# Kernel optimization log

Measured on AMD Instinct MI355X. Metric: run time of the kernel, lower is better.

## Reference

```python
import jax, jax.numpy as jnp
import numpy as np

B, T, HID = 4, 2048, 1024
H, FD, HD = 16, 16, 64          # heads, feature_dim, head_dim
CHUNK = 64                      # chunk size for chunked linear attention
EPS_LN = 1e-5                   # layer-norm eps inside feature map
EPS_Z = 1e-10                   # normalize_output eps


def setup_inputs() -> dict:
    key = jax.random.key(0)
    ks = jax.random.split(key, 7)
    init = lambda k, shp: jax.random.normal(k, shp, jnp.float32) * (shp[-1] ** -0.5)
    return {
        "hidden_states": jax.random.normal(ks[0], (B, T, HID), jnp.float32),
        "Wq": init(ks[1], (H * FD, HID)),     # q_proj weight [out,in], no bias
        "Wk": init(ks[2], (H * FD, HID)),
        "Wv": init(ks[3], (H * HD, HID)),
        "Wo": init(ks[4], (H * HD, HID)),
        "gamma": jnp.ones((FD,), jnp.float32),  # RebasedFeatureMap layer-norm scale
        "beta": jnp.zeros((FD,), jnp.float32),  # RebasedFeatureMap layer-norm shift
    }


def _feature_map(x, gamma, beta):
    # layer_norm over feature_dim, then quadratic (outer-product) feature map.
    mu = x.mean(-1, keepdims=True)
    var = ((x - mu) ** 2).mean(-1, keepdims=True)
    xn = (x - mu) * jax.lax.rsqrt(var + EPS_LN) * gamma + beta
    d = xn.shape[-1]
    # [B,T,H,d] -> [B,T,H,d*d]
    x2 = (xn[..., :, None] * xn[..., None, :]).reshape(*xn.shape[:-1], d * d)
    return x2 * (d ** -0.5)


def _chunk_linear_attn(q, k, v):
    # Chunk-recurrent causal linear attention (simple GLA with no gates, scale=1).
    Bq, Tq, Hq, Kq = q.shape
    Vd = v.shape[-1]
    N = Tq // CHUNK
    # [B,T,H,D] -> [N,B,H,C,D] for scan over chunks
    to_chunks = lambda x: x.reshape(Bq, N, CHUNK, Hq, x.shape[-1]).transpose(1, 0, 3, 2, 4)
    qc, kc, vc = to_chunks(q), to_chunks(k), to_chunks(v)
    mask = jnp.tril(jnp.ones((CHUNK, CHUNK), bool))

    def step(state, xs):
        qb, kb, vb = xs  # [B,H,C,K], [B,H,C,K], [B,H,C,V]
        att = jnp.einsum('bhik,bhjk->bhij', qb, kb)
        att = jnp.where(mask, att, 0.0)
        o = jnp.einsum('bhij,bhjv->bhiv', att, vb) + jnp.einsum('bhik,bhkv->bhiv', qb, state)
        state = state + jnp.einsum('bhck,bhcv->bhkv', kb, vb)
        return state, o

    state0 = jnp.zeros((Bq, Hq, Kq, Vd), q.dtype)
    _, o = jax.lax.scan(step, state0, (qc, kc, vc))  # o: [N,B,H,C,V]
    o = o.transpose(1, 0, 3, 2, 4).reshape(Bq, Tq, Hq, Vd)
    # normalize_output: z_t = q_t . cumsum_{s<=t} k_s
    z = jnp.einsum('bthk,bthk->bth', q, jnp.cumsum(k, axis=1))[..., None]
    return o / (z + EPS_Z)


def reference(hidden_states, Wq, Wk, Wv, Wo, gamma, beta):
    Bh, Th, _ = hidden_states.shape
    q = (hidden_states @ Wq.T).reshape(Bh, Th, H, FD)
    k = (hidden_states @ Wk.T).reshape(Bh, Th, H, FD)
    v = (hidden_states @ Wv.T).reshape(Bh, Th, H, HD)
    qf = _feature_map(q, gamma, beta)  # [B,T,H,FD*FD]
    kf = _feature_map(k, gamma, beta)
    o = _chunk_linear_attn(qf, kf, v)  # [B,T,H,HD]
    o = o.reshape(Bh, Th, H * HD)
    return o @ Wo.T
```

## Files before the change

kernel.cpp:

```cpp
#include <hip/hip_runtime.h>

#define T_SEQ 2048
#define BATCH 4
#define NH 16
#define FDIM 16
#define HDIM 64
#define HIDDEN 1024
#define TOK (BATCH * T_SEQ)
#define CH 128
#define NCHUNK (T_SEQ / CH)
#define NBH (BATCH * NH)

#define QK_OFF   0u
#define VT_OFF   4194304u
#define SRAW_OFF 8388608u
#define SPRE_OFF 16777216u
#define MK_OFF   25165824u
#define OAB_OFF  25427968u
#define WQKV_OFF 29622272u
#define WO_OFF   30408704u
#define HSB_OFF  30932992u

typedef float f32x4 __attribute__((ext_vector_type(4)));
typedef short bf16x8 __attribute__((ext_vector_type(8)));
typedef unsigned short us8 __attribute__((ext_vector_type(8)));
typedef unsigned short us4 __attribute__((ext_vector_type(4)));
typedef unsigned int u32;

__device__ __forceinline__ unsigned short f2b(float f) {
  union { float f; unsigned u; } v; v.f = f;
  unsigned r = (v.u + 0x7FFFu + ((v.u >> 16) & 1u)) >> 16;
  return (unsigned short)r;
}
__device__ __forceinline__ float b2f(unsigned short h) {
  union { unsigned u; float f; } v; v.u = ((unsigned)h) << 16; return v.f;
}

__device__ __forceinline__ void gload_lds16(const void* g, void* l) {
  __builtin_amdgcn_global_load_lds(
      (const __attribute__((address_space(1))) u32*)g,
      (__attribute__((address_space(3))) u32*)l, 16, 0, 0);
}

__global__ __launch_bounds__(256) void conv_all(const float* __restrict__ hs,
                                                const float* __restrict__ Wq,
                                                const float* __restrict__ Wk,
                                                const float* __restrict__ Wv,
                                                const float* __restrict__ Wo,
                                                unsigned short* __restrict__ HSB,
                                                unsigned short* __restrict__ WQKVB,
                                                unsigned short* __restrict__ WOB) {
  int i = blockIdx.x * 256 + threadIdx.x;
  const float* src;
  unsigned short* dst;
  if (i < 1048576) {
    int f = i * 8; src = hs + f; dst = HSB + f;
  } else if (i < 1245184) {
    int f = (i - 1048576) * 8;
    if (f < 262144)      src = Wq + f;
    else if (f < 524288) src = Wk + (f - 262144);
    else                 src = Wv + (f - 524288);
    dst = WQKVB + f;
  } else {
    int f = (i - 1245184) * 8;
    src = Wo + f; dst = WOB + f;
  }
  float4 v0 = *(const float4*)src, v1 = *(const float4*)(src + 4);
  us8 o;
  o[0] = f2b(v0.x); o[1] = f2b(v0.y); o[2] = f2b(v0.z); o[3] = f2b(v0.w);
  o[4] = f2b(v1.x); o[5] = f2b(v1.y); o[6] = f2b(v1.z); o[7] = f2b(v1.w);
  *(us8*)dst = o;
}

#define LDSA(p) (lds + (p) * 8192)
#define LDSB(p) (lds + 16384 + (p) * 8192)

__device__ __forceinline__ void stage8(const unsigned short* __restrict__ A,
                                       const unsigned short* __restrict__ B,
                                       int m0, int n0, int kt,
                                       unsigned short* lA, unsigned short* lB,
                                       int w, int lrow, int kswz) {
  const int kc = kt * 64 + kswz;
#pragma unroll
  for (int i = 0; i < 4; ++i) {
    int r = w * 32 + i * 8;
    gload_lds16(&A[(size_t)(m0 + r + lrow) * HIDDEN + kc], &lA[r * 64]);
  }
#pragma unroll
  for (int i = 0; i < 4; ++i) {
    int r = w * 32 + i * 8;
    gload_lds16(&B[(size_t)(n0 + r + lrow) * HIDDEN + kc], &lB[r * 64]);
  }
}

#define RD_A(fm, kk) (*(const bf16x8*)&cA[(wm * 64 + (fm) * 16 + ln) * 64 + (((kk) * 32 + lg * 8) ^ swz)])
#define RD_B(fn, kk) (*(const bf16x8*)&cB[(wn * 64 + (fn) * 16 + ln) * 64 + (((kk) * 32 + lg * 8) ^ swz)])

#define GEMM_PIPELINE(Aptr, Bptr)                                              \
  const int tid = threadIdx.x;                                                 \
  const int lane = tid & 63, w = tid >> 6;                                     \
  const int wm = w >> 1, wn = w & 1;                                           \
  const int ln = lane & 15, lg = lane >> 4;                                    \
  const int lrow = lane >> 3;                                                  \
  const int kswz = (((lane & 7) ^ ((lane >> 3) & 7)) * 8);                     \
  const int swz = (ln & 7) << 3;                                               \
  f32x4 acc[4][4];                                                             \
  _Pragma("unroll") for (int m = 0; m < 4; ++m)                                \
    _Pragma("unroll") for (int n = 0; n < 4; ++n)                              \
      acc[m][n] = (f32x4){0.f, 0.f, 0.f, 0.f};                                 \
  stage8(Aptr, Bptr, m0, n0, 0, LDSA(0), LDSB(0), w, lrow, kswz);              \
  stage8(Aptr, Bptr, m0, n0, 1, LDSA(1), LDSB(1), w, lrow, kswz);              \
  asm volatile("s_waitcnt vmcnt(8)" ::: "memory");                             \
  __builtin_amdgcn_s_barrier();                                                \
  _Pragma("unroll 1") for (int t = 0; t < 16; ++t) {                           \
    const unsigned short* cA = LDSA(t & 1);                                    \
    const unsigned short* cB = LDSB(t & 1);                                    \
    bf16x8 af[4][2], bfr[4][2];                                                \
    _Pragma("unroll") for (int f = 0; f < 4; ++f) {                            \
      af[f][0] = RD_A(f, 0); af[f][1] = RD_A(f, 1);                            \
      bfr[f][0] = RD_B(f, 0); bfr[f][1] = RD_B(f, 1);                          \
    }                                                                          \
    asm volatile("s_waitcnt lgkmcnt(0)" ::: "memory");                         \
    __builtin_amdgcn_sched_barrier(0);                                         \
    __builtin_amdgcn_s_barrier();                                              \
    if (t <= 13)                                                               \
      stage8(Aptr, Bptr, m0, n0, t + 2, LDSA(t & 1), LDSB(t & 1), w, lrow, kswz); \
    __builtin_amdgcn_s_setprio(1);                                             \
    _Pragma("unroll") for (int kk = 0; kk < 2; ++kk)                           \
      _Pragma("unroll") for (int fm = 0; fm < 4; ++fm)                         \
        _Pragma("unroll") for (int fn = 0; fn < 4; ++fn)                       \
          acc[fm][fn] = __builtin_amdgcn_mfma_f32_16x16x32_bf16(               \
              af[fm][kk], bfr[fn][kk], acc[fm][fn], 0, 0, 0);                  \
    __builtin_amdgcn_s_setprio(0);                                             \
    if (t <= 13) { asm volatile("s_waitcnt vmcnt(8)" ::: "memory"); }          \
    else if (t == 14) { asm volatile("s_waitcnt vmcnt(0)" ::: "memory"); }     \
    __builtin_amdgcn_s_barrier();                                              \
  }

__global__ __launch_bounds__(256) void proj_gemm(const unsigned short* __restrict__ A,
                                                 const unsigned short* __restrict__ Wb,
                                                 float* __restrict__ QK,
                                                 unsigned short* __restrict__ VTg) {
  __shared__ unsigned short lds[32768];
  const int bid = blockIdx.x;
  const int logical = (bid & 7) * 96 + (bid >> 3);
  const int bx = logical / 12, by = logical % 12;
  const int m0 = bx * 128, n0 = by * 128;

  GEMM_PIPELINE(A, Wb)

  if (by < 4) {
#pragma unroll
    for (int fm = 0; fm < 4; ++fm)
#pragma unroll
      for (int fn = 0; fn < 4; ++fn) {
        int col = n0 + wn * 64 + fn * 16 + ln;
        int row0 = m0 + wm * 64 + fm * 16 + lg * 4;
#pragma unroll
        for (int j = 0; j < 4; ++j)
          QK[(size_t)(row0 + j) * 512 + col] = acc[fm][fn][j];
      }
  } else {
    unsigned short (*ct)[136] = (unsigned short(*)[136])lds;
#pragma unroll
    for (int fm = 0; fm < 4; ++fm)
#pragma unroll
      for (int fn = 0; fn < 4; ++fn) {
        int cl = wn * 64 + fn * 16 + ln;
        int r0 = wm * 64 + fm * 16 + lg * 4;
        us4 p;
#pragma unroll
        for (int j = 0; j < 4; ++j) p[j] = f2b(acc[fm][fn][j]);
        *(us4*)&ct[cl][r0] = p;
      }
    __builtin_amdgcn_s_barrier();
    asm volatile("" ::: "memory");
    const int vbase = n0 - 512;
    const int b = m0 >> 11, t0 = m0 & 2047;
#pragma unroll
    for (int it = 0; it < 8; ++it) {
      int sid = it * 256 + tid, vl = sid >> 4, tc = sid & 15;
      int vg = vbase + vl, h = vg >> 6, vd = vg & 63;
      us8 val = *(const us8*)&ct[vl][tc * 8];
      *(us8*)&VTg[(((size_t)(b * 16 + h) * 64 + vd) << 11) + t0 + tc * 8] = val;
    }
  }
}

__global__ __launch_bounds__(256) void out_gemm(const unsigned short* __restrict__ A,
                                                const unsigned short* __restrict__ W,
                                                float* __restrict__ C) {
  __shared__ unsigned short lds[32768];
  const int bid = blockIdx.x;
  const int logical = (bid & 7) * 64 + (bid >> 3);
  const int bx = logical >> 3, by = logical & 7;
  const int m0 = bx * 128, n0 = by * 128;

  GEMM_PIPELINE(A, W)

#pragma unroll
  for (int fm = 0; fm < 4; ++fm)
#pragma unroll
    for (int fn = 0; fn < 4; ++fn) {
      int col = n0 + wn * 64 + fn * 16 + ln;
      int row0 = m0 + wm * 64 + fm * 16 + lg * 4;
#pragma unroll
      for (int j = 0; j < 4; ++j)
        C[(size_t)(row0 + j) * 1024 + col] = acc[fm][fn][j];
    }
}

__device__ __forceinline__ void ln16(const float* __restrict__ src,
                                     const float* __restrict__ gamma,
                                     const float* __restrict__ beta,
                                     float* dst) {
  float x[16];
#pragma unroll
  for (int q = 0; q < 4; ++q) {
    float4 v = *(const float4*)(src + q * 4);
    x[q * 4 + 0] = v.x; x[q * 4 + 1] = v.y;
    x[q * 4 + 2] = v.z; x[q * 4 + 3] = v.w;
  }
  float mu = 0.f;
#pragma unroll
  for (int f = 0; f < 16; ++f) mu += x[f];
  mu *= 0.0625f;
  float var = 0.f;
#pragma unroll
  for (int f = 0; f < 16; ++f) { float d = x[f] - mu; var += d * d; }
  var *= 0.0625f;
  const float rs = rsqrtf(var + 1e-5f);
#pragma unroll
  for (int f = 0; f < 16; ++f) dst[f] = (x[f] - mu) * rs * gamma[f] + beta[f];
}

__global__ __launch_bounds__(256) void k_states(const float* __restrict__ QK,
                                                const unsigned short* __restrict__ VTg,
                                                const float* __restrict__ gamma,
                                                const float* __restrict__ beta,
                                                unsigned short* __restrict__ Sraw,
                                                float* __restrict__ Mk) {
  const int c = blockIdx.x, bh = blockIdx.y;
  const int b = bh >> 4, h = bh & 15;
  __shared__ float XKT[16][140];
  __shared__ unsigned short VT[64][152];
  const int tid = threadIdx.x;
  const int lane = tid & 63, wid = tid >> 6;
  const int ln = lane & 15, lg = lane >> 4;

  if (tid < 128) {
    float xr[16];
    ln16(QK + (size_t)(b * T_SEQ + c * CH + tid) * 512 + 256 + h * FDIM, gamma, beta, xr);
#pragma unroll
    for (int f = 0; f < 16; ++f) XKT[f][tid] = xr[f];
  }
#pragma unroll
  for (int it = 0; it < 4; ++it) {
    int flat = tid + it * 256; int v = flat >> 4, sb = flat & 15;
    *(us8*)&VT[v][sb * 8] = *(const us8*)&VTg[((size_t)bh * 64 + v) * T_SEQ + c * CH + sb * 8];
  }
  __syncthreads();

  {
    int i = tid >> 4, j = tid & 15;
    float m = 0.f;
    for (int cc = 0; cc < CH; ++cc) m += XKT[i][cc] * XKT[j][cc];
    Mk[((size_t)bh * NCHUNK + c) * 256 + tid] = m;
  }

  f32x4 acc[4][4];
#pragma unroll
  for (int m = 0; m < 4; ++m)
#pragma unroll
    for (int n = 0; n < 4; ++n) acc[m][n] = (f32x4){0.f, 0.f, 0.f, 0.f};

#pragma unroll
  for (int kt = 0; kt < 4; ++kt) {
    const int s0 = kt * 32 + lg * 8;
    bf16x8 bfr[4];
#pragma unroll
    for (int nt = 0; nt < 4; ++nt) bfr[nt] = *(const bf16x8*)&VT[nt * 16 + ln][s0];
#pragma unroll
    for (int mi = 0; mi < 4; ++mi) {
      const int iidx = wid * 4 + mi;
      float4 xi0 = *(const float4*)&XKT[iidx][s0];
      float4 xi1 = *(const float4*)&XKT[iidx][s0 + 4];
      float4 xj0 = *(const float4*)&XKT[ln][s0];
      float4 xj1 = *(const float4*)&XKT[ln][s0 + 4];
      bf16x8 afr;
      afr[0] = (short)f2b(xi0.x * xj0.x); afr[1] = (short)f2b(xi0.y * xj0.y);
      afr[2] = (short)f2b(xi0.z * xj0.z); afr[3] = (short)f2b(xi0.w * xj0.w);
      afr[4] = (short)f2b(xi1.x * xj1.x); afr[5] = (short)f2b(xi1.y * xj1.y);
      afr[6] = (short)f2b(xi1.z * xj1.z); afr[7] = (short)f2b(xi1.w * xj1.w);
#pragma unroll
      for (int nt = 0; nt < 4; ++nt)
        acc[mi][nt] = __builtin_amdgcn_mfma_f32_16x16x32_bf16(afr, bfr[nt], acc[mi][nt], 0, 0, 0);
    }
  }

  unsigned short* Sp = Sraw + ((size_t)bh * NCHUNK + c) * (64 * 256);
#pragma unroll
  for (int mi = 0; mi < 4; ++mi) {
    int r0 = (wid * 4 + mi) * 16 + lg * 4;
#pragma unroll
    for (int nt = 0; nt < 4; ++nt) {
      int n = nt * 16 + ln;
      us4 pk;
#pragma unroll
      for (int j = 0; j < 4; ++j) pk[j] = f2b(acc[mi][nt][j]);
      *(us4*)&Sp[(size_t)n * 256 + r0] = pk;
    }
  }
}

__global__ __launch_bounds__(256) void k_prefix(const unsigned short* __restrict__ Sraw,
                                                unsigned short* __restrict__ Spre,
                                                float* __restrict__ Mk) {
  const int bh = blockIdx.y;
  if (blockIdx.x < 8) {
    const int e8 = blockIdx.x * 256 + threadIdx.x;
    size_t base = (size_t)bh * NCHUNK * 16384 + (size_t)e8 * 8;
    float run[8] = {0.f, 0.f, 0.f, 0.f, 0.f, 0.f, 0.f, 0.f};
    for (int cc = 0; cc < NCHUNK; ++cc) {
      us8 v = *(const us8*)&Sraw[base + (size_t)cc * 16384];
      us8 w;
#pragma unroll
      for (int q = 0; q < 8; ++q) w[q] = f2b(run[q]);
      *(us8*)&Spre[base + (size_t)cc * 16384] = w;
#pragma unroll
      for (int q = 0; q < 8; ++q) run[q] += b2f(v[q]);
    }
  } else {
    const int e = threadIdx.x;
    size_t base = (size_t)bh * NCHUNK * 256 + e;
    float run = 0.f;
    for (int c = 0; c < NCHUNK; ++c) {
      float v = Mk[base + (size_t)c * 256];
      Mk[base + (size_t)c * 256] = run;
      run += v;
    }
  }
}

__global__ __launch_bounds__(256) void k_attn_out(const float* __restrict__ QK,
                                                  const unsigned short* __restrict__ VTg,
                                                  const float* __restrict__ gamma,
                                                  const float* __restrict__ beta,
                                                  const unsigned short* __restrict__ Spre,
                                                  const float* __restrict__ Mkp,
                                                  unsigned short* __restrict__ OAB) {
  const int c = blockIdx.x, bh = blockIdx.y;
  const int b = bh >> 4, h = bh & 15;
  __shared__ unsigned short XQb[128][40];
  __shared__ unsigned short XKb[128][40];
  __shared__ unsigned short attb[128 * 128];
  __shared__ unsigned short VT[64][152];
  __shared__ float mksh[256];
  const int tid = threadIdx.x;
  const int lane = tid & 63, wid = tid >> 6;
  const int ln = lane & 15, lg = lane >> 4;

  {
    int r = tid & 127;
    const float* src = QK + (size_t)(b * T_SEQ + c * CH + r) * 512 + (tid < 128 ? 0 : 256) + h * FDIM;
    unsigned short* dst = (tid < 128) ? &XQb[r][0] : &XKb[r][0];
    float xr[16];
    ln16(src, gamma, beta, xr);
    us8 lo, hi, z8;
#pragma unroll
    for (int q = 0; q < 8; ++q) { lo[q] = f2b(xr[q]); hi[q] = f2b(xr[8 + q]); z8[q] = 0; }
    *(us8*)&dst[0] = lo; *(us8*)&dst[8] = hi;
    *(us8*)&dst[16] = z8; *(us8*)&dst[24] = z8;
  }
#pragma unroll
  for (int it = 0; it < 4; ++it) {
    int flat = tid + it * 256; int v = flat >> 4, sb = flat & 15;
    *(us8*)&VT[v][sb * 8] = *(const us8*)&VTg[((size_t)bh * 64 + v) * T_SEQ + c * CH + sb * 8];
  }
  mksh[tid] = Mkp[((size_t)bh * NCHUNK + c) * 256 + tid];
  __syncthreads();

  const int tb = wid * 32;
  const f32x4 zero4 = {0.f, 0.f, 0.f, 0.f};

  bf16x8 aq0 = *(const bf16x8*)&XQb[tb + ln][lg * 8];
  bf16x8 aq1 = *(const bf16x8*)&XQb[tb + 16 + ln][lg * 8];
  float zin[2][4];
#pragma unroll
  for (int mt = 0; mt < 2; ++mt)
#pragma unroll
    for (int j = 0; j < 4; ++j) zin[mt][j] = 0.f;

#pragma unroll
  for (int nt = 0; nt < 8; ++nt) {
    bf16x8 bk = *(const bf16x8*)&XKb[nt * 16 + ln][lg * 8];
    f32x4 c0 = __builtin_amdgcn_mfma_f32_16x16x32_bf16(aq0, bk, zero4, 0, 0, 0);
    f32x4 c1 = __builtin_amdgcn_mfma_f32_16x16x32_bf16(aq1, bk, zero4, 0, 0, 0);
    int s = nt * 16 + ln;
#pragma unroll
    for (int j = 0; j < 4; ++j) {
      int t0 = tb + lg * 4 + j;
      float d0 = c0[j];
      float a0 = (s <= t0) ? d0 * d0 * 0.0625f : 0.f;
      zin[0][j] += a0;
      attb[t0 * 128 + (s ^ ((t0 & 7) << 3))] = f2b(a0);
      int t1 = t0 + 16;
      float d1 = c1[j];
      float a1 = (s <= t1) ? d1 * d1 * 0.0625f : 0.f;
      zin[1][j] += a1;
      attb[t1 * 128 + (s ^ ((t1 & 7) << 3))] = f2b(a1);
    }
  }
#pragma unroll
  for (int mt = 0; mt < 2; ++mt)
#pragma unroll
    for (int j = 0; j < 4; ++j) {
      float zz = zin[mt][j];
      zz += __shfl_xor(zz, 1, 64);
      zz += __shfl_xor(zz, 2, 64);
      zz += __shfl_xor(zz, 4, 64);
      zz += __shfl_xor(zz, 8, 64);
      zin[mt][j] = zz;
    }

  f32x4 o[2][4];
#pragma unroll
  for (int mt = 0; mt < 2; ++mt)
#pragma unroll
    for (int nt = 0; nt < 4; ++nt) o[mt][nt] = zero4;

#pragma unroll
  for (int kt = 0; kt < 4; ++kt) {
    int s0 = kt * 32 + lg * 8;
    bf16x8 a0 = *(const bf16x8*)&attb[(tb + ln) * 128 + (s0 ^ ((ln & 7) << 3))];
    bf16x8 a1 = *(const bf16x8*)&attb[(tb + 16 + ln) * 128 + (s0 ^ ((ln & 7) << 3))];
#pragma unroll
    for (int nt = 0; nt < 4; ++nt) {
      bf16x8 bv = *(const bf16x8*)&VT[nt * 16 + ln][s0];
      o[0][nt] = __builtin_amdgcn_mfma_f32_16x16x32_bf16(a0, bv, o[0][nt], 0, 0, 0);
      o[1][nt] = __builtin_amdgcn_mfma_f32_16x16x32_bf16(a1, bv, o[1][nt], 0, 0, 0);
    }
  }

  const unsigned short* Sp = Spre + ((size_t)bh * NCHUNK + c) * (64 * 256);
  bf16x8 xlo0 = *(const bf16x8*)&XQb[tb + ln][0];
  bf16x8 xhi0 = *(const bf16x8*)&XQb[tb + ln][8];
  bf16x8 xlo1 = *(const bf16x8*)&XQb[tb + 16 + ln][0];
  bf16x8 xhi1 = *(const bf16x8*)&XQb[tb + 16 + ln][8];
#pragma unroll
  for (int kt = 0; kt < 8; ++kt) {
    int i = kt * 2 + (lg >> 1);
    float xqi0 = b2f(XQb[tb + ln][i]) * 0.0625f;
    float xqi1 = b2f(XQb[tb + 16 + ln][i]) * 0.0625f;
    bf16x8 sel0 = (lg & 1) ? xhi0 : xlo0;
    bf16x8 sel1 = (lg & 1) ? xhi1 : xlo1;
    bf16x8 qa0, qa1;
#pragma unroll
    for (int jj = 0; jj < 8; ++jj) {
      qa0[jj] = (short)f2b(xqi0 * b2f((unsigned short)sel0[jj]));
      qa1[jj] = (short)f2b(xqi1 * b2f((unsigned short)sel1[jj]));
    }
    int r0 = kt * 32 + lg * 8;
#pragma unroll
    for (int nt = 0; nt < 4; ++nt) {
      bf16x8 bp = *(const bf16x8*)&Sp[(size_t)(nt * 16 + ln) * 256 + r0];
      o[0][nt] = __builtin_amdgcn_mfma_f32_16x16x32_bf16(qa0, bp, o[0][nt], 0, 0, 0);
      o[1][nt] = __builtin_amdgcn_mfma_f32_16x16x32_bf16(qa1, bp, o[1][nt], 0, 0, 0);
    }
  }

  float zi2[2][4];
#pragma unroll
  for (int mt = 0; mt < 2; ++mt)
#pragma unroll
    for (int j = 0; j < 4; ++j) {
      int t = tb + mt * 16 + lg * 4 + j;
      float xqi = b2f(XQb[t][ln]);
      float p = 0.f;
#pragma unroll
      for (int jm = 0; jm < 16; ++jm) p += b2f(XQb[t][jm]) * mksh[jm * 16 + ln];
      p *= xqi;
      p += __shfl_xor(p, 1, 64);
      p += __shfl_xor(p, 2, 64);
      p += __shfl_xor(p, 4, 64);
      p += __shfl_xor(p, 8, 64);
      zi2[mt][j] = p * 0.0625f;
    }

  unsigned short* ob = OAB + ((size_t)(b * T_SEQ + c * CH)) * 1024 + h * 64;
#pragma unroll
  for (int mt = 0; mt < 2; ++mt)
#pragma unroll
    for (int j = 0; j < 4; ++j) {
      int t = tb + mt * 16 + lg * 4 + j;
      float inv = 1.0f / (zin[mt][j] + zi2[mt][j] + 1e-10f);
#pragma unroll
      for (int nt = 0; nt < 4; ++nt)
        ob[(size_t)t * 1024 + nt * 16 + ln] = f2b(o[mt][nt][j] * inv);
    }
}

extern "C" void kernel_launch(void* const* d_in, const int* in_sizes, int n_in,
                              void* d_out, int out_size, void* d_ws, size_t ws_size,
                              hipStream_t stream) {
  const float* hs    = (const float*)d_in[0];
  const float* Wq    = (const float*)d_in[1];
  const float* Wk    = (const float*)d_in[2];
  const float* Wv    = (const float*)d_in[3];
  const float* Wo    = (const float*)d_in[4];
  const float* gamma = (const float*)d_in[5];
  const float* beta  = (const float*)d_in[6];
  float* out = (float*)d_out;
  float* ws  = (float*)d_ws;

  float* QK = ws + QK_OFF;
  unsigned short* VTg   = (unsigned short*)(ws + VT_OFF);
  unsigned short* Sraw  = (unsigned short*)(ws + SRAW_OFF);
  unsigned short* Spre  = (unsigned short*)(ws + SPRE_OFF);
  float* Mk = ws + MK_OFF;
  unsigned short* OAB   = (unsigned short*)(ws + OAB_OFF);
  unsigned short* WQKVB = (unsigned short*)(ws + WQKV_OFF);
  unsigned short* WOB   = (unsigned short*)(ws + WO_OFF);
  unsigned short* HSB   = (unsigned short*)(ws + HSB_OFF);

  dim3 blk(256);
  conv_all<<<5376, blk, 0, stream>>>(hs, Wq, Wk, Wv, Wo, HSB, WQKVB, WOB);
  proj_gemm<<<768, blk, 0, stream>>>(HSB, WQKVB, QK, VTg);
  k_states<<<dim3(NCHUNK, NBH), blk, 0, stream>>>(QK, VTg, gamma, beta, Sraw, Mk);
  k_prefix<<<dim3(9, NBH), blk, 0, stream>>>(Sraw, Spre, Mk);
  k_attn_out<<<dim3(NCHUNK, NBH), blk, 0, stream>>>(QK, VTg, gamma, beta, Spre, Mk, OAB);
  out_gemm<<<512, blk, 0, stream>>>(OAB, WOB, out);
}
```

Baseline: 127.4 us.

## Fuse chunk-state computation and prefix scan into one sequential per-head kernel

Replaces the separate per-chunk state kernel and the prefix-sum kernel with one kernel. Each block owns a (batch-head, 16-column V slice) and walks the chunks sequentially, accumulating the running state in MFMA registers and writing the exclusive prefix directly. This removes the Sraw round trip through global memory and one launch, and double-buffers the K features and V tiles in shared memory to overlap loads with compute. In exchange, parallelism drops to 256 blocks that each run a serial 16-step loop, and the Mk prefix is computed redundantly by only the vs==0 blocks.

```diff
diff --git a/kernel.cpp b/kernel.cpp
--- a/kernel.cpp
+++ b/kernel.cpp
@@ -13,7 +13,6 @@
 
 #define QK_OFF   0u
 #define VT_OFF   4194304u
-#define SRAW_OFF 8388608u
 #define SPRE_OFF 16777216u
 #define MK_OFF   25165824u
 #define OAB_OFF  25427968u
@@ -210,135 +209,133 @@
     }
 }
 
+__device__ __forceinline__ void ln16_reg(float4 a0, float4 a1, float4 a2, float4 a3,
+                                         const float* __restrict__ gamma,
+                                         const float* __restrict__ beta,
+                                         float* dst) {
+  float x[16] = {a0.x, a0.y, a0.z, a0.w, a1.x, a1.y, a1.z, a1.w,
+                 a2.x, a2.y, a2.z, a2.w, a3.x, a3.y, a3.z, a3.w};
+  float mu = 0.f;
+#pragma unroll
+  for (int f = 0; f < 16; ++f) mu += x[f];
+  mu *= 0.0625f;
+  float var = 0.f;
+#pragma unroll
+  for (int f = 0; f < 16; ++f) { float d = x[f] - mu; var += d * d; }
+  var *= 0.0625f;
+  const float rs = rsqrtf(var + 1e-5f);
+#pragma unroll
+  for (int f = 0; f < 16; ++f) dst[f] = (x[f] - mu) * rs * gamma[f] + beta[f];
+}
+
 __device__ __forceinline__ void ln16(const float* __restrict__ src,
                                      const float* __restrict__ gamma,
                                      const float* __restrict__ beta,
                                      float* dst) {
-  float x[16];
-#pragma unroll
-  for (int q = 0; q < 4; ++q) {
-    float4 v = *(const float4*)(src + q * 4);
-    x[q * 4 + 0] = v.x; x[q * 4 + 1] = v.y;
-    x[q * 4 + 2] = v.z; x[q * 4 + 3] = v.w;
-  }
-  float mu = 0.f;
-#pragma unroll
-  for (int f = 0; f < 16; ++f) mu += x[f];
-  mu *= 0.0625f;
-  float var = 0.f;
-#pragma unroll
-  for (int f = 0; f < 16; ++f) { float d = x[f] - mu; var += d * d; }
-  var *= 0.0625f;
-  const float rs = rsqrtf(var + 1e-5f);
-#pragma unroll
-  for (int f = 0; f < 16; ++f) dst[f] = (x[f] - mu) * rs * gamma[f] + beta[f];
-}
-
-__global__ __launch_bounds__(256) void k_states(const float* __restrict__ QK,
-                                                const unsigned short* __restrict__ VTg,
-                                                const float* __restrict__ gamma,
-                                                const float* __restrict__ beta,
-                                                unsigned short* __restrict__ Sraw,
-                                                float* __restrict__ Mk) {
-  const int c = blockIdx.x, bh = blockIdx.y;
+  float4 a0 = *(const float4*)(src + 0);
+  float4 a1 = *(const float4*)(src + 4);
+  float4 a2 = *(const float4*)(src + 8);
+  float4 a3 = *(const float4*)(src + 12);
+  ln16_reg(a0, a1, a2, a3, gamma, beta, dst);
+}
+
+__global__ __launch_bounds__(256) void k_state_prefix(const float* __restrict__ QK,
+                                                      const unsigned short* __restrict__ VTg,
+                                                      const float* __restrict__ gamma,
+                                                      const float* __restrict__ beta,
+                                                      unsigned short* __restrict__ Spre,
+                                                      float* __restrict__ Mk) {
+  const int vs = blockIdx.x, bh = blockIdx.y;
   const int b = bh >> 4, h = bh & 15;
-  __shared__ float XKT[16][140];
-  __shared__ unsigned short VT[64][152];
+  __shared__ float XKT[2][16][140];
+  __shared__ unsigned short VT[2][16][136];
   const int tid = threadIdx.x;
   const int lane = tid & 63, wid = tid >> 6;
   const int ln = lane & 15, lg = lane >> 4;
-
+  const int vrow = tid >> 4, vcol = (tid & 15) * 8;
+
+  f32x4 state[4];
+#pragma unroll
+  for (int m = 0; m < 4; ++m) state[m] = (f32x4){0.f, 0.f, 0.f, 0.f};
+  float mkrun = 0.f;
+
+  float4 xq0, xq1, xq2, xq3;
+  us8 vtr;
+  if (tid < 128) {
+    const float* src = QK + (size_t)(b * T_SEQ + tid) * 512 + 256 + h * FDIM;
+    xq0 = *(const float4*)(src + 0);  xq1 = *(const float4*)(src + 4);
+    xq2 = *(const float4*)(src + 8);  xq3 = *(const float4*)(src + 12);
+  }
+  vtr = *(const us8*)&VTg[((size_t)bh * 64 + vs * 16 + vrow) * T_SEQ + vcol];
   if (tid < 128) {
     float xr[16];
-    ln16(QK + (size_t)(b * T_SEQ + c * CH + tid) * 512 + 256 + h * FDIM, gamma, beta, xr);
-#pragma unroll
-    for (int f = 0; f < 16; ++f) XKT[f][tid] = xr[f];
-  }
-#pragma unroll
-  for (int it = 0; it < 4; ++it) {
-    int flat = tid + it * 256; int v = flat >> 4, sb = flat & 15;
-    *(us8*)&VT[v][sb * 8] = *(const us8*)&VTg[((size_t)bh * 64 + v) * T_SEQ + c * CH + sb * 8];
-  }
+    ln16_reg(xq0, xq1, xq2, xq3, gamma, beta, xr);
+#pragma unroll
+    for (int f = 0; f < 16; ++f) XKT[0][f][tid] = xr[f];
+  }
+  *(us8*)&VT[0][vrow][vcol] = vtr;
   __syncthreads();
 
-  {
-    int i = tid >> 4, j = tid & 15;
-    float m = 0.f;
-    for (int cc = 0; cc < CH; ++cc) m += XKT[i][cc] * XKT[j][cc];
-    Mk[((size_t)bh * NCHUNK + c) * 256 + tid] = m;
-  }
-
-  f32x4 acc[4][4];
-#pragma unroll
-  for (int m = 0; m < 4; ++m)
-#pragma unroll
-    for (int n = 0; n < 4; ++n) acc[m][n] = (f32x4){0.f, 0.f, 0.f, 0.f};
-
-#pragma unroll
-  for (int kt = 0; kt < 4; ++kt) {
-    const int s0 = kt * 32 + lg * 8;
-    bf16x8 bfr[4];
-#pragma unroll
-    for (int nt = 0; nt < 4; ++nt) bfr[nt] = *(const bf16x8*)&VT[nt * 16 + ln][s0];
+  for (int c = 0; c < NCHUNK; ++c) {
+    const int pb = c & 1;
+    if (c < NCHUNK - 1) {
+      if (tid < 128) {
+        const float* src = QK + (size_t)(b * T_SEQ + (c + 1) * CH + tid) * 512 + 256 + h * FDIM;
+        xq0 = *(const float4*)(src + 0);  xq1 = *(const float4*)(src + 4);
+        xq2 = *(const float4*)(src + 8);  xq3 = *(const float4*)(src + 12);
+      }
+      vtr = *(const us8*)&VTg[((size_t)bh * 64 + vs * 16 + vrow) * T_SEQ + (c + 1) * CH + vcol];
+    }
+
+    unsigned short* Sp = Spre + ((size_t)bh * NCHUNK + c) * (64 * 256);
 #pragma unroll
     for (int mi = 0; mi < 4; ++mi) {
-      const int iidx = wid * 4 + mi;
-      float4 xi0 = *(const float4*)&XKT[iidx][s0];
-      float4 xi1 = *(const float4*)&XKT[iidx][s0 + 4];
-      float4 xj0 = *(const float4*)&XKT[ln][s0];
-      float4 xj1 = *(const float4*)&XKT[ln][s0 + 4];
-      bf16x8 afr;
-      afr[0] = (short)f2b(xi0.x * xj0.x); afr[1] = (short)f2b(xi0.y * xj0.y);
-      afr[2] = (short)f2b(xi0.z * xj0.z); afr[3] = (short)f2b(xi0.w * xj0.w);
-      afr[4] = (short)f2b(xi1.x * xj1.x); afr[5] = (short)f2b(xi1.y * xj1.y);
-      afr[6] = (short)f2b(xi1.z * xj1.z); afr[7] = (short)f2b(xi1.w * xj1.w);
-#pragma unroll
-      for (int nt = 0; nt < 4; ++nt)
-        acc[mi][nt] = __builtin_amdgcn_mfma_f32_16x16x32_bf16(afr, bfr[nt], acc[mi][nt], 0, 0, 0);
-    }
-  }
-
-  unsigned short* Sp = Sraw + ((size_t)bh * NCHUNK + c) * (64 * 256);
-#pragma unroll
-  for (int mi = 0; mi < 4; ++mi) {
-    int r0 = (wid * 4 + mi) * 16 + lg * 4;
-#pragma unroll
-    for (int nt = 0; nt < 4; ++nt) {
-      int n = nt * 16 + ln;
+      int r0 = (wid * 4 + mi) * 16 + lg * 4;
       us4 pk;
 #pragma unroll
-      for (int j = 0; j < 4; ++j) pk[j] = f2b(acc[mi][nt][j]);
-      *(us4*)&Sp[(size_t)n * 256 + r0] = pk;
-    }
-  }
-}
-
-__global__ __launch_bounds__(256) void k_prefix(const unsigned short* __restrict__ Sraw,
-                                                unsigned short* __restrict__ Spre,
-                                                float* __restrict__ Mk) {
-  const int bh = blockIdx.y;
-  if (blockIdx.x < 8) {
-    const int e8 = blockIdx.x * 256 + threadIdx.x;
-    size_t base = (size_t)bh * NCHUNK * 16384 + (size_t)e8 * 8;
-    float run[8] = {0.f, 0.f, 0.f, 0.f, 0.f, 0.f, 0.f, 0.f};
-    for (int cc = 0; cc < NCHUNK; ++cc) {
-      us8 v = *(const us8*)&Sraw[base + (size_t)cc * 16384];
-      us8 w;
-#pragma unroll
-      for (int q = 0; q < 8; ++q) w[q] = f2b(run[q]);
-      *(us8*)&Spre[base + (size_t)cc * 16384] = w;
-#pragma unroll
-      for (int q = 0; q < 8; ++q) run[q] += b2f(v[q]);
-    }
-  } else {
-    const int e = threadIdx.x;
-    size_t base = (size_t)bh * NCHUNK * 256 + e;
-    float run = 0.f;
-    for (int c = 0; c < NCHUNK; ++c) {
-      float v = Mk[base + (size_t)c * 256];
-      Mk[base + (size_t)c * 256] = run;
-      run += v;
-    }
+      for (int j = 0; j < 4; ++j) pk[j] = f2b(state[mi][j]);
+      *(us4*)&Sp[(size_t)(vs * 16 + ln) * 256 + r0] = pk;
+    }
+    if (vs == 0) Mk[((size_t)bh * NCHUNK + c) * 256 + tid] = mkrun;
+
+    if (vs == 0) {
+      int i = tid >> 4, j = tid & 15;
+      float m = 0.f;
+#pragma unroll
+      for (int cc = 0; cc < CH; ++cc) m += XKT[pb][i][cc] * XKT[pb][j][cc];
+      mkrun += m;
+    }
+
+#pragma unroll
+    for (int kt = 0; kt < 4; ++kt) {
+      const int s0 = kt * 32 + lg * 8;
+      bf16x8 bfr = *(const bf16x8*)&VT[pb][ln][s0];
+#pragma unroll
+      for (int mi = 0; mi < 4; ++mi) {
+        const int iidx = wid * 4 + mi;
+        float4 xi0 = *(const float4*)&XKT[pb][iidx][s0];
+        float4 xi1 = *(const float4*)&XKT[pb][iidx][s0 + 4];
+        float4 xj0 = *(const float4*)&XKT[pb][ln][s0];
+        float4 xj1 = *(const float4*)&XKT[pb][ln][s0 + 4];
+        bf16x8 afr;
+        afr[0] = (short)f2b(xi0.x * xj0.x); afr[1] = (short)f2b(xi0.y * xj0.y);
+        afr[2] = (short)f2b(xi0.z * xj0.z); afr[3] = (short)f2b(xi0.w * xj0.w);
+        afr[4] = (short)f2b(xi1.x * xj1.x); afr[5] = (short)f2b(xi1.y * xj1.y);
+        afr[6] = (short)f2b(xi1.z * xj1.z); afr[7] = (short)f2b(xi1.w * xj1.w);
+        state[mi] = __builtin_amdgcn_mfma_f32_16x16x32_bf16(afr, bfr, state[mi], 0, 0, 0);
+      }
+    }
+
+    if (c < NCHUNK - 1) {
+      if (tid < 128) {
+        float xr[16];
+        ln16_reg(xq0, xq1, xq2, xq3, gamma, beta, xr);
+#pragma unroll
+        for (int f = 0; f < 16; ++f) XKT[pb ^ 1][f][tid] = xr[f];
+      }
+      *(us8*)&VT[pb ^ 1][vrow][vcol] = vtr;
+    }
+    __syncthreads();
   }
 }
 
@@ -515,7 +512,6 @@
 
   float* QK = ws + QK_OFF;
   unsigned short* VTg   = (unsigned short*)(ws + VT_OFF);
-  unsigned short* Sraw  = (unsigned short*)(ws + SRAW_OFF);
   unsigned short* Spre  = (unsigned short*)(ws + SPRE_OFF);
   float* Mk = ws + MK_OFF;
   unsigned short* OAB   = (unsigned short*)(ws + OAB_OFF);
@@ -526,8 +522,7 @@
   dim3 blk(256);
   conv_all<<<5376, blk, 0, stream>>>(hs, Wq, Wk, Wv, Wo, HSB, WQKVB, WOB);
   proj_gemm<<<768, blk, 0, stream>>>(HSB, WQKVB, QK, VTg);
-  k_states<<<dim3(NCHUNK, NBH), blk, 0, stream>>>(QK, VTg, gamma, beta, Sraw, Mk);
-  k_prefix<<<dim3(9, NBH), blk, 0, stream>>>(Sraw, Spre, Mk);
+  k_state_prefix<<<dim3(4, NBH), blk, 0, stream>>>(QK, VTg, gamma, beta, Spre, Mk);
   k_attn_out<<<dim3(NCHUNK, NBH), blk, 0, stream>>>(QK, VTg, gamma, beta, Spre, Mk, OAB);
   out_gemm<<<512, blk, 0, stream>>>(OAB, WOB, out);
 }
```

Result: slower. 144.1 us (+13.1%).
